# Optimization experiments

Measured on AMD Instinct MI355X. Metric: run time of the kernel, lower is better.

Reference implementation:

```python
import jax, jax.numpy as jnp
import numpy as np

H = 512

def setup_inputs() -> dict:
    key = jax.random.key(0)
    k1, k2, k3 = jax.random.split(key, 3)
    encoder_outputs = jax.random.normal(k1, (32, 4096, H), dtype=jnp.float32)  # (B,T,H)
    W = jax.random.normal(k2, (H, H), dtype=jnp.float32) * (1.0 / np.sqrt(H))  # attn.weight
    v = jax.random.normal(k3, (H,), dtype=jnp.float32) * (1.0 / np.sqrt(H))    # v param
    return {"encoder_outputs": encoder_outputs, "W": W, "v": v}

def reference(encoder_outputs, W, v):
    # score: energy = tanh(x @ W.T); attn_energies = v . energy over H -> (B,T)
    energy = jnp.tanh(jnp.einsum('bth,gh->btg', encoder_outputs, W))
    attn_energies = jnp.einsum('btg,g->bt', energy, v)
    # method == 'bmm': softmax over T, weighted sum over T -> (B,H)
    attn_w = jax.nn.softmax(attn_energies, axis=-1)
    out = jnp.einsum('bt,bth->bh', attn_w, encoder_outputs)
    return out
```

## Files before the change

### kernel.cpp

```cpp
#include <hip/hip_runtime.h>
#include <hip/hip_bf16.h>

typedef __attribute__((ext_vector_type(8))) short short8;
typedef __attribute__((ext_vector_type(4))) float f32x4;

#define B_SZ 32
#define T_SZ 4096
#define H_SZ 512
#define NROWS (B_SZ * T_SZ)

static __device__ __forceinline__ unsigned int pack2(float a, float b) {
  unsigned int r;
  asm("v_cvt_pk_bf16_f32 %0, %1, %2" : "=v"(r) : "v"(a), "v"(b));
  return r;
}

static __device__ __forceinline__ float fast_tanh(float x) {
  float e = __expf(2.0f * x);
  return 1.0f - 2.0f / (e + 1.0f);
}

__global__ __launch_bounds__(256) void prep_w_kernel(
    const float* __restrict__ W, uint4* __restrict__ Wfrag) {
  int s = blockIdx.x * 256 + threadIdx.x;
  int grow  = s >> 6;
  int kt    = (s >> 2) & 15;
  int kslot = s & 3;
  const float4* Wf4 = reinterpret_cast<const float4*>(W);
  float4 lo = Wf4[grow * 128 + kt * 8 + kslot * 2];
  float4 hi = Wf4[grow * 128 + kt * 8 + kslot * 2 + 1];
  uint4 u;
  u.x = pack2(lo.x, lo.y); u.y = pack2(lo.z, lo.w);
  u.z = pack2(hi.x, hi.y); u.w = pack2(hi.z, hi.w);
  int nb = grow >> 4, g = grow & 15;
  Wfrag[nb * 1024 + kt * 64 + kslot * 16 + g] = u;
}

__global__ __launch_bounds__(256, 2) void score_fused_kernel(
    const float* __restrict__ X, const uint4* __restrict__ Wfrag,
    const float* __restrict__ v,
    float* __restrict__ num, float2* __restrict__ md) {
  __shared__ unsigned char WsB[3][16384];
  __shared__ float vLDS[512];
  __shared__ float sLDS[128];
  __shared__ float pLDS[128];
  __shared__ float mred[2], dred[2];

  const int tid   = threadIdx.x;
  const int lane  = tid & 63;
  const int wave  = tid >> 6;
  const int frow  = lane & 15;
  const int kslot = lane >> 4;
  const size_t rowbase = (size_t)blockIdx.x * 128;

  #define STAGE(c)                                                              \
    {                                                                           \
      const char* src = (const char*)Wfrag + (size_t)(c) * 16384 +              \
                        wave * 4096 + lane * 16;                                \
      unsigned char* dst = &WsB[(c) % 3][wave * 4096];                          \
      _Pragma("unroll")                                                         \
      for (int i = 0; i < 4; ++i)                                               \
        __builtin_amdgcn_global_load_lds((const unsigned int*)(src + i * 1024), \
                                         (unsigned int*)(dst + i * 1024), 16, 0, 0); \
    }

  STAGE(0);
  STAGE(1);
  reinterpret_cast<float2*>(vLDS)[tid] = reinterpret_cast<const float2*>(v)[tid];

  short8 afrag0[16], afrag1[16];
  {
    const float4* xr0 = reinterpret_cast<const float4*>(X + (rowbase + wave * 32 + frow) * H_SZ);
    const float4* xr1 = reinterpret_cast<const float4*>(X + (rowbase + wave * 32 + 16 + frow) * H_SZ);
    #pragma unroll
    for (int kt = 0; kt < 16; ++kt) {
      float4 lo0 = xr0[kt * 8 + kslot * 2];
      float4 hi0 = xr0[kt * 8 + kslot * 2 + 1];
      union { uint4 u; short8 s; } c0;
      c0.u.x = pack2(lo0.x, lo0.y); c0.u.y = pack2(lo0.z, lo0.w);
      c0.u.z = pack2(hi0.x, hi0.y); c0.u.w = pack2(hi0.z, hi0.w);
      afrag0[kt] = c0.s;
      float4 lo1 = xr1[kt * 8 + kslot * 2];
      float4 hi1 = xr1[kt * 8 + kslot * 2 + 1];
      union { uint4 u; short8 s; } c1;
      c1.u.x = pack2(lo1.x, lo1.y); c1.u.y = pack2(lo1.z, lo1.w);
      c1.u.z = pack2(hi1.x, hi1.y); c1.u.w = pack2(hi1.z, hi1.w);
      afrag1[kt] = c1.s;
    }
  }
  asm volatile("s_waitcnt vmcnt(0) lgkmcnt(0)" ::: "memory");
  __builtin_amdgcn_s_barrier();
  __builtin_amdgcn_sched_barrier(0);

  float red0[4] = {0.f, 0.f, 0.f, 0.f};
  float red1[4] = {0.f, 0.f, 0.f, 0.f};

  f32x4 accP[2][2];
  float vgP = 0.f;

  for (int ch = 0; ch < 32; ++ch) {
    if (ch + 2 < 32) STAGE(ch + 2);
    float vg = vLDS[ch * 16 + frow];

    f32x4 accC[2][2];
    #pragma unroll
    for (int a = 0; a < 2; ++a)
      #pragma unroll
      for (int p = 0; p < 2; ++p)
        accC[a][p] = (f32x4){0.f, 0.f, 0.f, 0.f};

    const unsigned char* bb = &WsB[ch % 3][lane * 16];
    #pragma unroll
    for (int kt = 0; kt < 16; ++kt) {
      short8 b = *reinterpret_cast<const short8*>(bb + kt * 1024);
      const int p = kt & 1;
      accC[0][p] = __builtin_amdgcn_mfma_f32_16x16x32_bf16(afrag0[kt], b, accC[0][p], 0, 0, 0);
      accC[1][p] = __builtin_amdgcn_mfma_f32_16x16x32_bf16(afrag1[kt], b, accC[1][p], 0, 0, 0);
    }

    if (ch > 0) {
      #pragma unroll
      for (int r = 0; r < 4; ++r) {
        red0[r] = fmaf(vgP, fast_tanh(accP[0][0][r] + accP[0][1][r]), red0[r]);
        red1[r] = fmaf(vgP, fast_tanh(accP[1][0][r] + accP[1][1][r]), red1[r]);
      }
    }
    #pragma unroll
    for (int a = 0; a < 2; ++a)
      #pragma unroll
      for (int p = 0; p < 2; ++p)
        accP[a][p] = accC[a][p];
    vgP = vg;

    if (ch < 31) {
      if (ch < 30) {
        asm volatile("s_waitcnt vmcnt(4)" ::: "memory");
      } else {
        asm volatile("s_waitcnt vmcnt(0)" ::: "memory");
      }
      __builtin_amdgcn_s_barrier();
      __builtin_amdgcn_sched_barrier(0);
    }
  }
  #undef STAGE

  #pragma unroll
  for (int r = 0; r < 4; ++r) {
    red0[r] = fmaf(vgP, fast_tanh(accP[0][0][r] + accP[0][1][r]), red0[r]);
    red1[r] = fmaf(vgP, fast_tanh(accP[1][0][r] + accP[1][1][r]), red1[r]);
  }

  #pragma unroll
  for (int r = 0; r < 4; ++r) {
    #pragma unroll
    for (int d = 1; d < 16; d <<= 1) {
      red0[r] += __shfl_xor(red0[r], d);
      red1[r] += __shfl_xor(red1[r], d);
    }
  }
  if (frow == 0) {
    float* sp = sLDS + wave * 32 + kslot * 4;
    sp[0]  = red0[0]; sp[1]  = red0[1]; sp[2]  = red0[2]; sp[3]  = red0[3];
    sp[16] = red1[0]; sp[17] = red1[1]; sp[18] = red1[2]; sp[19] = red1[3];
  }
  __syncthreads();

  if (tid < 128) {
    float s = sLDS[tid];
    float m = s;
    #pragma unroll
    for (int d = 1; d < 64; d <<= 1) m = fmaxf(m, __shfl_xor(m, d));
    if ((tid & 63) == 0) mred[tid >> 6] = m;
  }
  __syncthreads();
  const float m_loc = fmaxf(mred[0], mred[1]);
  if (tid < 128) {
    float p = __expf(sLDS[tid] - m_loc);
    pLDS[tid] = p;
    #pragma unroll
    for (int d = 1; d < 64; d <<= 1) p += __shfl_xor(p, d);
    if ((tid & 63) == 0) dred[tid >> 6] = p;
  }
  __syncthreads();

  {
    float ax = 0.f, ay = 0.f;
    const float2* xb = reinterpret_cast<const float2*>(X + rowbase * H_SZ) + tid;
    #pragma unroll 8
    for (int t = 0; t < 128; ++t) {
      float p = pLDS[t];
      float2 xv = xb[(size_t)t * (H_SZ / 2)];
      ax = fmaf(p, xv.x, ax);
      ay = fmaf(p, xv.y, ay);
    }
    float2 r; r.x = ax; r.y = ay;
    reinterpret_cast<float2*>(num + (size_t)blockIdx.x * H_SZ)[tid] = r;
  }
  if (tid == 0) {
    float2 r; r.x = m_loc; r.y = dred[0] + dred[1];
    md[blockIdx.x] = r;
  }
}

__global__ __launch_bounds__(512) void combine_kernel(
    const float* __restrict__ num, const float2* __restrict__ md,
    float* __restrict__ out) {
  const int b = blockIdx.x;
  const int h = threadIdx.x;
  float M = -1e30f;
  #pragma unroll
  for (int c = 0; c < 32; ++c) M = fmaxf(M, md[b * 32 + c].x);
  float den = 0.f, acc = 0.f;
  #pragma unroll 4
  for (int c = 0; c < 32; ++c) {
    float2 m2 = md[b * 32 + c];
    float w = __expf(m2.x - M);
    den += w * m2.y;
    acc = fmaf(w, num[(size_t)(b * 32 + c) * H_SZ + h], acc);
  }
  out[b * H_SZ + h] = acc / den;
}

extern "C" void kernel_launch(void* const* d_in, const int* in_sizes, int n_in,
                              void* d_out, int out_size, void* d_ws, size_t ws_size,
                              hipStream_t stream) {
  const float* X = (const float*)d_in[0];
  const float* W = (const float*)d_in[1];
  const float* v = (const float*)d_in[2];
  float* out = (float*)d_out;
  unsigned char* ws = (unsigned char*)d_ws;

  uint4* Wfrag = (uint4*)(ws);
  float* num   = (float*)(ws + (512u << 10));
  float2* md   = (float2*)(ws + (512u << 10) + (2u << 20));

  prep_w_kernel<<<128, 256, 0, stream>>>(W, Wfrag);
  score_fused_kernel<<<NROWS / 128, 256, 0, stream>>>(X, Wfrag, v, num, md);
  combine_kernel<<<B_SZ, 512, 0, stream>>>(num, md, out);
}
```

Baseline: 163.9 us.

## Interleave W chunk staging with MFMA phases using barriers and setprio

Splits each 16 KB W-chunk prefetch into four per-phase global_load_lds issues, one inside each of four MFMA phases per chunk. Each phase is bracketed by workgroup barriers and s_setprio raises, aiming to spread memory issue across the compute and let waves alternate between load and MFMA work. The deferred tanh/v reduction of the previous chunk is dropped in favour of an immediate epilogue per chunk, which simplifies register use but loses that overlap. The extra barriers per chunk add synchronisation cost.

```diff
diff --git a/kernel.cpp b/kernel.cpp
--- a/kernel.cpp
+++ b/kernel.cpp
@@ -53,19 +53,19 @@
   const int kslot = lane >> 4;
   const size_t rowbase = (size_t)blockIdx.x * 128;
 
-  #define STAGE(c)                                                              \
+  #define STAGE_RD(c, p)                                                        \
     {                                                                           \
       const char* src = (const char*)Wfrag + (size_t)(c) * 16384 +              \
-                        wave * 4096 + lane * 16;                                \
-      unsigned char* dst = &WsB[(c) % 3][wave * 4096];                          \
-      _Pragma("unroll")                                                         \
-      for (int i = 0; i < 4; ++i)                                               \
-        __builtin_amdgcn_global_load_lds((const unsigned int*)(src + i * 1024), \
-                                         (unsigned int*)(dst + i * 1024), 16, 0, 0); \
-    }
-
-  STAGE(0);
-  STAGE(1);
+                        (p) * 4096 + wave * 1024 + lane * 16;                   \
+      unsigned char* dst = &WsB[(c) % 3][(p) * 4096 + wave * 1024];             \
+      __builtin_amdgcn_global_load_lds((const unsigned int*)src,                \
+                                       (unsigned int*)dst, 16, 0, 0);           \
+    }
+
+  #pragma unroll
+  for (int p = 0; p < 4; ++p) STAGE_RD(0, p);
+  #pragma unroll
+  for (int p = 0; p < 4; ++p) STAGE_RD(1, p);
   reinterpret_cast<float2*>(vLDS)[tid] = reinterpret_cast<const float2*>(v)[tid];
 
   short8 afrag0[16], afrag1[16];
@@ -88,49 +88,56 @@
       afrag1[kt] = c1.s;
     }
   }
-  asm volatile("s_waitcnt vmcnt(0) lgkmcnt(0)" ::: "memory");
+  asm volatile("s_waitcnt vmcnt(4) lgkmcnt(0)" ::: "memory");
   __builtin_amdgcn_s_barrier();
   __builtin_amdgcn_sched_barrier(0);
 
   float red0[4] = {0.f, 0.f, 0.f, 0.f};
   float red1[4] = {0.f, 0.f, 0.f, 0.f};
 
-  f32x4 accP[2][2];
-  float vgP = 0.f;
-
   for (int ch = 0; ch < 32; ++ch) {
-    if (ch + 2 < 32) STAGE(ch + 2);
+    const int stage_c = ch + 2;
+    const unsigned char* bb = &WsB[ch % 3][lane * 16];
     float vg = vLDS[ch * 16 + frow];
 
-    f32x4 accC[2][2];
+    f32x4 acc[2][2];
     #pragma unroll
     for (int a = 0; a < 2; ++a)
       #pragma unroll
       for (int p = 0; p < 2; ++p)
-        accC[a][p] = (f32x4){0.f, 0.f, 0.f, 0.f};
-
-    const unsigned char* bb = &WsB[ch % 3][lane * 16];
-    #pragma unroll
-    for (int kt = 0; kt < 16; ++kt) {
-      short8 b = *reinterpret_cast<const short8*>(bb + kt * 1024);
-      const int p = kt & 1;
-      accC[0][p] = __builtin_amdgcn_mfma_f32_16x16x32_bf16(afrag0[kt], b, accC[0][p], 0, 0, 0);
-      accC[1][p] = __builtin_amdgcn_mfma_f32_16x16x32_bf16(afrag1[kt], b, accC[1][p], 0, 0, 0);
-    }
-
-    if (ch > 0) {
-      #pragma unroll
-      for (int r = 0; r < 4; ++r) {
-        red0[r] = fmaf(vgP, fast_tanh(accP[0][0][r] + accP[0][1][r]), red0[r]);
-        red1[r] = fmaf(vgP, fast_tanh(accP[1][0][r] + accP[1][1][r]), red1[r]);
+        acc[a][p] = (f32x4){0.f, 0.f, 0.f, 0.f};
+
+    #pragma unroll
+    for (int ph = 0; ph < 4; ++ph) {
+      short8 b0 = *reinterpret_cast<const short8*>(bb + (ph * 4 + 0) * 1024);
+      short8 b1 = *reinterpret_cast<const short8*>(bb + (ph * 4 + 1) * 1024);
+      short8 b2 = *reinterpret_cast<const short8*>(bb + (ph * 4 + 2) * 1024);
+      short8 b3 = *reinterpret_cast<const short8*>(bb + (ph * 4 + 3) * 1024);
+      if (stage_c < 32) STAGE_RD(stage_c, ph);
+      __builtin_amdgcn_s_barrier();
+      __builtin_amdgcn_sched_barrier(0);
+      __builtin_amdgcn_s_setprio(1);
+      {
+        const int k0 = ph * 4;
+        acc[0][(k0 + 0) & 1] = __builtin_amdgcn_mfma_f32_16x16x32_bf16(afrag0[k0 + 0], b0, acc[0][(k0 + 0) & 1], 0, 0, 0);
+        acc[1][(k0 + 0) & 1] = __builtin_amdgcn_mfma_f32_16x16x32_bf16(afrag1[k0 + 0], b0, acc[1][(k0 + 0) & 1], 0, 0, 0);
+        acc[0][(k0 + 1) & 1] = __builtin_amdgcn_mfma_f32_16x16x32_bf16(afrag0[k0 + 1], b1, acc[0][(k0 + 1) & 1], 0, 0, 0);
+        acc[1][(k0 + 1) & 1] = __builtin_amdgcn_mfma_f32_16x16x32_bf16(afrag1[k0 + 1], b1, acc[1][(k0 + 1) & 1], 0, 0, 0);
+        acc[0][(k0 + 2) & 1] = __builtin_amdgcn_mfma_f32_16x16x32_bf16(afrag0[k0 + 2], b2, acc[0][(k0 + 2) & 1], 0, 0, 0);
+        acc[1][(k0 + 2) & 1] = __builtin_amdgcn_mfma_f32_16x16x32_bf16(afrag1[k0 + 2], b2, acc[1][(k0 + 2) & 1], 0, 0, 0);
+        acc[0][(k0 + 3) & 1] = __builtin_amdgcn_mfma_f32_16x16x32_bf16(afrag0[k0 + 3], b3, acc[0][(k0 + 3) & 1], 0, 0, 0);
+        acc[1][(k0 + 3) & 1] = __builtin_amdgcn_mfma_f32_16x16x32_bf16(afrag1[k0 + 3], b3, acc[1][(k0 + 3) & 1], 0, 0, 0);
       }
-    }
-    #pragma unroll
-    for (int a = 0; a < 2; ++a)
-      #pragma unroll
-      for (int p = 0; p < 2; ++p)
-        accP[a][p] = accC[a][p];
-    vgP = vg;
+      __builtin_amdgcn_s_setprio(0);
+      __builtin_amdgcn_s_barrier();
+      __builtin_amdgcn_sched_barrier(0);
+    }
+
+    #pragma unroll
+    for (int r = 0; r < 4; ++r) {
+      red0[r] = fmaf(vg, fast_tanh(acc[0][0][r] + acc[0][1][r]), red0[r]);
+      red1[r] = fmaf(vg, fast_tanh(acc[1][0][r] + acc[1][1][r]), red1[r]);
+    }
 
     if (ch < 31) {
       if (ch < 30) {
@@ -142,13 +149,7 @@
       __builtin_amdgcn_sched_barrier(0);
     }
   }
-  #undef STAGE
-
-  #pragma unroll
-  for (int r = 0; r < 4; ++r) {
-    red0[r] = fmaf(vgP, fast_tanh(accP[0][0][r] + accP[0][1][r]), red0[r]);
-    red1[r] = fmaf(vgP, fast_tanh(accP[1][0][r] + accP[1][1][r]), red1[r]);
-  }
+  #undef STAGE_RD
 
   #pragma unroll
   for (int r = 0; r < 4; ++r) {
```

Result: no change. 163.6 us (-0.1%).
